# Optimization experiments

Hardware: AMD Instinct MI355X
Metric: run time of the kernel (lower is better)

The kernel has to match this reference:

```python
import jax, jax.numpy as jnp
import numpy as np

D_MODEL = 512
WINDOW_SIZE = 257


def setup_inputs() -> dict:
    key = jax.random.key(0)
    ks = jax.random.split(key, 7)
    B, S, D = 4, 4096, D_MODEL
    scale = 1.0 / np.sqrt(D)
    return {
        "x": jax.random.normal(ks[0], (B, S, D), dtype=jnp.float32),
        "Wq": jax.random.normal(ks[1], (D, D), dtype=jnp.float32) * scale,
        "bq": jnp.zeros((D,), dtype=jnp.float32),
        "Wk": jax.random.normal(ks[2], (D, D), dtype=jnp.float32) * scale,
        "bk": jnp.zeros((D,), dtype=jnp.float32),
        "Wv": jax.random.normal(ks[3], (D, D), dtype=jnp.float32) * scale,
        "bv": jnp.zeros((D,), dtype=jnp.float32),
    }


def reference(x, Wq, bq, Wk, bk, Wv, bv):
    B, S, D = x.shape
    half_window = (WINDOW_SIZE - 1) // 2
    Q = x @ Wq + bq
    K = x @ Wk + bk
    V = x @ Wv + bv
    # full [B,S,S] scores, then band mask |i-j| <= half_window (matches original)
    scores = jnp.einsum("bsd,btd->bst", Q, K) / jnp.sqrt(jnp.asarray(D, x.dtype))
    idx = jnp.arange(S)
    local_mask = jnp.abs(idx[:, None] - idx[None, :]) <= half_window  # [S,S]
    scores = jnp.where(local_mask[None], scores, -jnp.inf)
    attn = jax.nn.softmax(scores, axis=-1)
    return jnp.einsum("bst,btd->bsd", attn, V)
```

## Files before the change

### kernel.cpp

```cpp
#include <hip/hip_runtime.h>
#include <hip/hip_bf16.h>

#define S_LEN   4096
#define D_MOD   512
#define BATCH   4
#define HALF_W  128
#define M_TOT   (BATCH * S_LEN)

typedef __attribute__((ext_vector_type(8))) short bf16x8;
typedef __attribute__((ext_vector_type(4))) float f32x4;

__device__ __forceinline__ unsigned short f2bf(float f) {
    unsigned int u = __float_as_uint(f);
    unsigned int r = (u + 0x7fffu + ((u >> 16) & 1u)) >> 16;
    return (unsigned short)r;
}

__device__ __forceinline__ void async_copy16(const void* g, void* l) {
    __builtin_amdgcn_global_load_lds(
        (const __attribute__((address_space(1))) void*)g,
        (__attribute__((address_space(3))) void*)l, 16, 0, 0);
}

__global__ __launch_bounds__(256) void convert_xw(const float* __restrict__ x,
                                                  const float* __restrict__ Wq,
                                                  const float* __restrict__ Wk,
                                                  const float* __restrict__ Wv,
                                                  unsigned short* __restrict__ xb,
                                                  unsigned short* __restrict__ Wt) {
    __shared__ float sT[64][65];
    const int t = threadIdx.x;
    const int bid = blockIdx.x;
    if (bid < 8192) {
        int i = (bid * 256 + t) * 4;
        float4 v = *(const float4*)(x + i);
        ushort4 o;
        o.x = f2bf(v.x); o.y = f2bf(v.y); o.z = f2bf(v.z); o.w = f2bf(v.w);
        *(ushort4*)(xb + i) = o;
        return;
    }
    const int j = bid - 8192;
    const int w = j >> 6;
    const int rj = j & 63;
    const float* W = (w == 0) ? Wq : ((w == 1) ? Wk : Wv);
    const int n0 = (rj & 7) * 64, k0 = (rj >> 3) * 64;
    const int r = t >> 4, c4 = (t & 15) * 4;
    #pragma unroll
    for (int i = 0; i < 4; ++i) {
        float4 v = *(const float4*)(W + (size_t)(k0 + r + i * 16) * 512 + n0 + c4);
        sT[c4 + 0][r + i * 16] = v.x;
        sT[c4 + 1][r + i * 16] = v.y;
        sT[c4 + 2][r + i * 16] = v.z;
        sT[c4 + 3][r + i * 16] = v.w;
    }
    __syncthreads();
    #pragma unroll
    for (int i = 0; i < 4; ++i) {
        int rr = (t >> 4) + i * 16;
        ushort4 o;
        o.x = f2bf(sT[rr][c4 + 0]);
        o.y = f2bf(sT[rr][c4 + 1]);
        o.z = f2bf(sT[rr][c4 + 2]);
        o.w = f2bf(sT[rr][c4 + 3]);
        *(ushort4*)(Wt + (size_t)w * 262144 + (size_t)(n0 + rr) * 512 + k0 + c4) = o;
    }
}

__global__ __launch_bounds__(512, 1) void qkv_gemm(
    const unsigned short* __restrict__ xb, const unsigned short* __restrict__ Wt,
    const float* __restrict__ bq, const float* __restrict__ bk, const float* __restrict__ bv,
    unsigned short* __restrict__ Qo, unsigned short* __restrict__ Ko,
    unsigned short* __restrict__ Vt) {
    __shared__ __align__(16) char gsmem[98304];
    unsigned short* const sA0 = (unsigned short*)gsmem;
    unsigned short* const sA1 = (unsigned short*)(gsmem + 32768);
    unsigned short* const sB0 = (unsigned short*)(gsmem + 65536);
    unsigned short* const sB1 = (unsigned short*)(gsmem + 81920);
    unsigned short* const sT  = (unsigned short*)gsmem;

    const int t = threadIdx.x;
    const int p = blockIdx.x;
    const int l = (p & 7) * 96 + (p >> 3);
    const int mi = l / 12;
    const int rzn = l - mi * 12;
    const int wsel = rzn >> 2;
    const int ni = rzn & 3;
    const int m0 = mi * 256;
    const int n0 = ni * 128;
    const unsigned short* Wb = Wt + (size_t)wsel * 262144;

    const int w = t >> 6, lane = t & 63;
    const int wm = (w & 3) * 64, wn = (w >> 2) * 64;
    const int qd = lane >> 4, l16 = lane & 15;

    f32x4 acc[4][4] = {};

    #pragma unroll
    for (int i = 0; i < 4; ++i) {
        int c = i * 512 + t;
        int row = c >> 3, cc = c & 7;
        int g = cc ^ (row & 7);
        async_copy16(xb + (size_t)(m0 + row) * 512 + g * 8, sA0 + c * 8);
    }
    #pragma unroll
    for (int i = 0; i < 2; ++i) {
        int c = i * 512 + t;
        int row = c >> 3, cc = c & 7;
        int g = cc ^ (row & 7);
        async_copy16(Wb + (size_t)(n0 + row) * 512 + g * 8, sB0 + c * 8);
    }
    __syncthreads();

    int cur = 0;
    for (int k0 = 0; k0 < 512; k0 += 64) {
        if (k0 + 64 < 512) {
            unsigned short* dA = cur ? sA0 : sA1;
            unsigned short* dB = cur ? sB0 : sB1;
            int k0n = k0 + 64;
            #pragma unroll
            for (int i = 0; i < 4; ++i) {
                int c = i * 512 + t;
                int row = c >> 3, cc = c & 7;
                int g = cc ^ (row & 7);
                async_copy16(xb + (size_t)(m0 + row) * 512 + k0n + g * 8, dA + c * 8);
            }
            #pragma unroll
            for (int i = 0; i < 2; ++i) {
                int c = i * 512 + t;
                int row = c >> 3, cc = c & 7;
                int g = cc ^ (row & 7);
                async_copy16(Wb + (size_t)(n0 + row) * 512 + k0n + g * 8, dB + c * 8);
            }
        }

        const unsigned short* sA = cur ? sA1 : sA0;
        const unsigned short* sB = cur ? sB1 : sB0;
        #pragma unroll
        for (int ks = 0; ks < 2; ++ks) {
            bf16x8 af[4], bfr[4];
            #pragma unroll
            for (int i = 0; i < 4; ++i) {
                int row = wm + i * 16 + l16;
                int ch = (ks * 4 + qd) ^ (row & 7);
                af[i] = *(const bf16x8*)(sA + row * 64 + ch * 8);
            }
            #pragma unroll
            for (int j = 0; j < 4; ++j) {
                int row = wn + j * 16 + l16;
                int ch = (ks * 4 + qd) ^ (row & 7);
                bfr[j] = *(const bf16x8*)(sB + row * 64 + ch * 8);
            }
            #pragma unroll
            for (int i = 0; i < 4; ++i)
                #pragma unroll
                for (int j = 0; j < 4; ++j)
                    acc[i][j] = __builtin_amdgcn_mfma_f32_16x16x32_bf16(af[i], bfr[j], acc[i][j], 0, 0, 0);
        }

        __syncthreads();
        cur ^= 1;
    }

    const float* bias = (wsel == 0) ? bq : ((wsel == 1) ? bk : bv);

    if (wsel < 2) {
        #pragma unroll
        for (int j = 0; j < 4; ++j) {
            int n = wn + j * 16 + l16;
            float bj = bias[n0 + n];
            #pragma unroll
            for (int i = 0; i < 4; ++i) {
                int mb = wm + i * 16 + qd * 4;
                #pragma unroll
                for (int r = 0; r < 4; ++r)
                    sT[(mb + r) * 136 + n] = f2bf(acc[i][j][r] + bj);
            }
        }
        __syncthreads();
        unsigned short* Og = (wsel == 0) ? Qo : Ko;
        #pragma unroll
        for (int i2 = 0; i2 < 4; ++i2)
            #pragma unroll
            for (int i3 = 0; i3 < 2; ++i3) {
                int m = i2 * 64 + (t >> 3);
                int ch = (t & 7) + i3 * 8;
                bf16x8 v = *(const bf16x8*)(sT + m * 136 + ch * 8);
                *(bf16x8*)(Og + (size_t)(m0 + m) * 512 + n0 + ch * 8) = v;
            }
    } else {
        #pragma unroll
        for (int j = 0; j < 4; ++j) {
            int n = wn + j * 16 + l16;
            float bj = bias[n0 + n];
            #pragma unroll
            for (int i = 0; i < 4; ++i) {
                int mb = wm + i * 16 + qd * 4;
                #pragma unroll
                for (int r = 0; r < 4; ++r)
                    sT[n * 264 + mb + r] = f2bf(acc[i][j][r] + bj);
            }
        }
        __syncthreads();
        #pragma unroll
        for (int i2 = 0; i2 < 2; ++i2)
            #pragma unroll
            for (int i3 = 0; i3 < 4; ++i3) {
                int n = i2 * 64 + (t >> 3);
                int ch = (t & 7) + i3 * 8;
                bf16x8 v = *(const bf16x8*)(sT + n * 264 + ch * 8);
                *(bf16x8*)(Vt + (size_t)(n0 + n) * M_TOT + m0 + ch * 8) = v;
            }
    }
}

__global__ __launch_bounds__(512, 2) void attn(const unsigned short* __restrict__ Qg,
                                               const unsigned short* __restrict__ Kg,
                                               const unsigned short* __restrict__ Vt,
                                               float* __restrict__ out) {
    __shared__ __align__(16) char smem[137472];
    unsigned short* const bK0 = (unsigned short*)(smem);
    unsigned short* const bK1 = (unsigned short*)(smem + 66048);
    unsigned short* const bV0 = (unsigned short*)(smem + 33280);
    unsigned short* const bV1 = (unsigned short*)(smem + 99328);
    unsigned short* const sQ  = (unsigned short*)(smem + 66048);
    unsigned short* const sP  = (unsigned short*)(smem + 132096);
    float* const lsum = (float*)(smem + 137216);

    const int t = threadIdx.x;
    const int p = blockIdx.x;
    const int l = (p & 7) * 32 + (p >> 3);
    const int q0 = (l & 63) * 64;
    const int b = l >> 6;
    const int bS = b * S_LEN;

    const int w = t >> 6, lane = t & 63;
    const int qd = lane >> 4, l16 = lane & 15;
    const int qs = w >> 1;
    const int qh = qs * 16;
    const int kh = (w & 1) * 16;
    const int dh = (w & 1) * 256;

    if (t < 64) lsum[t] = 0.f;

    const int kt_lo = (q0 < 128) ? ((128 - q0) >> 5) : 0;
    int kt_hi = (4192 - q0) >> 5;
    if (kt_hi > 9) kt_hi = 9;

    bf16x8 qreg[16];
    f32x4 oacc[16] = {};

    {
        int key0 = q0 - HALF_W + kt_lo * 32;
        #pragma unroll
        for (int i = 0; i < 4; ++i) {
            int c = i * 512 + t;
            int row = c >> 6, cc = c & 63;
            int rowg = key0 + row;
            rowg = (rowg < 0) ? 0 : ((rowg > S_LEN - 1) ? S_LEN - 1 : rowg);
            async_copy16(Kg + (size_t)(bS + rowg) * 512 + cc * 8, bK0 + row * 520 + cc * 8);
        }
        #pragma unroll
        for (int i = 0; i < 4; ++i) {
            int c = i * 512 + t;
            int rp = c >> 3, chs = c & 7;
            int ch = chs ^ (rp & 7);
            int d = rp * 2 + (ch >> 2);
            int kc = ch & 3;
            int kk = key0 + kc * 8;
            int koff = (kk >= 0 && kk + 8 <= S_LEN) ? kk : 0;
            async_copy16(Vt + (size_t)d * M_TOT + bS + koff, bV0 + c * 8);
        }
        #pragma unroll
        for (int i = 0; i < 8; ++i) {
            int c = i * 512 + t;
            int row = c >> 6, cc = c & 63;
            int g = cc ^ (row & 7);
            async_copy16(Qg + (size_t)(bS + q0 + row) * 512 + g * 8, sQ + row * 512 + cc * 8);
        }
    }
    asm volatile("s_waitcnt vmcnt(0)" ::: "memory");
    __builtin_amdgcn_s_barrier();
    #pragma unroll
    for (int c4 = 0; c4 < 4; ++c4)
        #pragma unroll
        for (int kc = 0; kc < 4; ++kc) {
            int chl = c4 * 16 + kc * 4 + qd;
            int chp = chl ^ (l16 & 7);
            qreg[c4 * 4 + kc] = *(const bf16x8*)(sQ + (qh + l16) * 512 + chp * 8);
        }
    asm volatile("s_waitcnt lgkmcnt(0)" ::: "memory");
    __builtin_amdgcn_s_barrier();

    int cur = 0;
    for (int kt = kt_lo; kt <= kt_hi; ++kt, cur ^= 1) {
        const int key0 = q0 - HALF_W + kt * 32;

        asm volatile("s_waitcnt vmcnt(0) lgkmcnt(0)" ::: "memory");
        __builtin_amdgcn_s_barrier();

        if (kt < kt_hi) {
            int key0n = key0 + 32;
            unsigned short* dK = cur ? bK0 : bK1;
            unsigned short* dV = cur ? bV0 : bV1;
            #pragma unroll
            for (int i = 0; i < 4; ++i) {
                int c = i * 512 + t;
                int row = c >> 6, cc = c & 63;
                int rowg = key0n + row;
                rowg = (rowg < 0) ? 0 : ((rowg > S_LEN - 1) ? S_LEN - 1 : rowg);
                async_copy16(Kg + (size_t)(bS + rowg) * 512 + cc * 8, dK + row * 520 + cc * 8);
            }
            #pragma unroll
            for (int i = 0; i < 4; ++i) {
                int c = i * 512 + t;
                int rp = c >> 3, chs = c & 7;
                int ch = chs ^ (rp & 7);
                int d = rp * 2 + (ch >> 2);
                int kc = ch & 3;
                int kk = key0n + kc * 8;
                int koff = (kk >= 0 && kk + 8 <= S_LEN) ? kk : 0;
                async_copy16(Vt + (size_t)d * M_TOT + bS + koff, dV + c * 8);
            }
        }

        const unsigned short* sK = cur ? bK1 : bK0;
        const unsigned short* sV = cur ? bV1 : bV0;

        f32x4 sacc = {0.f, 0.f, 0.f, 0.f};
        #pragma unroll
        for (int c4 = 0; c4 < 4; ++c4) {
            #pragma unroll
            for (int kc = 0; kc < 4; ++kc) {
                bf16x8 bk8 = *(const bf16x8*)(sK + (kh + l16) * 520 + c4 * 128 + kc * 32 + qd * 8);
                sacc = __builtin_amdgcn_mfma_f32_16x16x32_bf16(qreg[c4 * 4 + kc], bk8, sacc, 0, 0, 0);
            }
        }
        const float scale = 0.04419417382415922f;
        #pragma unroll
        for (int r = 0; r < 4; ++r) {
            int qi = q0 + qh + qd * 4 + r;
            int kj = key0 + kh + l16;
            bool valid = (kj >= 0) && (kj < S_LEN) && (kj >= qi - HALF_W) && (kj <= qi + HALF_W);
            float p2 = valid ? __expf(sacc[r] * scale) : 0.f;
            sP[(qh + qd * 4 + r) * 40 + kh + l16] = f2bf(p2);
            float s = p2;
            s += __shfl_xor(s, 1);
            s += __shfl_xor(s, 2);
            s += __shfl_xor(s, 4);
            s += __shfl_xor(s, 8);
            if (l16 == 0) atomicAdd(&lsum[qh + qd * 4 + r], s);
        }

        asm volatile("s_waitcnt lgkmcnt(0)" ::: "memory");
        __builtin_amdgcn_s_barrier();

        bf16x8 ap = *(const bf16x8*)(sP + (qh + l16) * 40 + qd * 8);
        #pragma unroll
        for (int dt = 0; dt < 16; ++dt) {
            int dv = dh + dt * 16 + l16;
            int rp = dv >> 1;
            int chs = (((dv & 1) << 2) + qd) ^ (rp & 7);
            bf16x8 bv8 = *(const bf16x8*)(sV + rp * 64 + chs * 8);
            oacc[dt] = __builtin_amdgcn_mfma_f32_16x16x32_bf16(ap, bv8, oacc[dt], 0, 0, 0);
        }
    }

    asm volatile("s_waitcnt lgkmcnt(0)" ::: "memory");
    __builtin_amdgcn_s_barrier();

    float inv[4];
    #pragma unroll
    for (int r = 0; r < 4; ++r)
        inv[r] = 1.0f / lsum[qh + qd * 4 + r];

    #pragma unroll
    for (int dt = 0; dt < 16; ++dt) {
        int dv = dh + dt * 16 + l16;
        #pragma unroll
        for (int r = 0; r < 4; ++r) {
            int q = qh + qd * 4 + r;
            out[(size_t)(bS + q0 + q) * 512 + dv] = oacc[dt][r] * inv[r];
        }
    }
}

extern "C" void kernel_launch(void* const* d_in, const int* in_sizes, int n_in,
                              void* d_out, int out_size, void* d_ws, size_t ws_size,
                              hipStream_t stream) {
    const float* x  = (const float*)d_in[0];
    const float* Wq = (const float*)d_in[1];
    const float* bq = (const float*)d_in[2];
    const float* Wk = (const float*)d_in[3];
    const float* bk = (const float*)d_in[4];
    const float* Wv = (const float*)d_in[5];
    const float* bv = (const float*)d_in[6];
    float* out = (float*)d_out;

    char* ws = (char*)d_ws;
    unsigned short* xb = (unsigned short*)(ws);
    unsigned short* Wt = (unsigned short*)(ws + 16777216);
    unsigned short* Qb = (unsigned short*)(ws + 18350080);
    unsigned short* Kb = (unsigned short*)(ws + 35127296);
    unsigned short* Vt = (unsigned short*)(ws + 51904512);

    convert_xw<<<8384, 256, 0, stream>>>(x, Wq, Wk, Wv, xb, Wt);
    qkv_gemm<<<768, 512, 0, stream>>>(xb, Wt, bq, bk, bv, Qb, Kb, Vt);
    attn<<<256, 512, 0, stream>>>(Qb, Kb, Vt, out);
}
```

Before: 157.3 us.

## Stage K/V tiles through registers with two-ahead prefetch instead of async LDS loads

Replaces the direct global-to-LDS async copies of K and V tiles with ordinary global loads into registers, which are then written to the alternate LDS buffer after each tile's compute. The prefetch now runs two tiles ahead, and the barrier moves to the end of the loop iteration. The aim is to hide global load latency behind the QK and PV MFMA work. In exchange it adds register pressure (8 extra bf16x8 vectors alongside 16 accumulators and 16 Q registers), explicit LDS store instructions, and reliance on compiler-inserted vmcnt waits.

```diff
diff --git a/kernel.cpp b/kernel.cpp
--- a/kernel.cpp
+++ b/kernel.cpp
@@ -246,8 +246,9 @@
     int kt_hi = (4192 - q0) >> 5;
     if (kt_hi > 9) kt_hi = 9;
 
-    bf16x8 qreg[16];
+    bf16x8 qreg[16], kreg[4], vreg[4];
     f32x4 oacc[16] = {};
+
 
     {
         int key0 = q0 - HALF_W + kt_lo * 32;
@@ -257,7 +258,7 @@
             int row = c >> 6, cc = c & 63;
             int rowg = key0 + row;
             rowg = (rowg < 0) ? 0 : ((rowg > S_LEN - 1) ? S_LEN - 1 : rowg);
-            async_copy16(Kg + (size_t)(bS + rowg) * 512 + cc * 8, bK0 + row * 520 + cc * 8);
+            kreg[i] = *(const bf16x8*)(Kg + (size_t)(bS + rowg) * 512 + cc * 8);
         }
         #pragma unroll
         for (int i = 0; i < 4; ++i) {
@@ -268,7 +269,7 @@
             int kc = ch & 3;
             int kk = key0 + kc * 8;
             int koff = (kk >= 0 && kk + 8 <= S_LEN) ? kk : 0;
-            async_copy16(Vt + (size_t)d * M_TOT + bS + koff, bV0 + c * 8);
+            vreg[i] = *(const bf16x8*)(Vt + (size_t)d * M_TOT + bS + koff);
         }
         #pragma unroll
         for (int i = 0; i < 8; ++i) {
@@ -291,38 +292,45 @@
     asm volatile("s_waitcnt lgkmcnt(0)" ::: "memory");
     __builtin_amdgcn_s_barrier();
 
+    #pragma unroll
+    for (int i = 0; i < 4; ++i) {
+        int c = i * 512 + t;
+        int row = c >> 6, cc = c & 63;
+        *(bf16x8*)(bK0 + row * 520 + cc * 8) = kreg[i];
+    }
+    #pragma unroll
+    for (int i = 0; i < 4; ++i) {
+        int c = i * 512 + t;
+        *(bf16x8*)(bV0 + c * 8) = vreg[i];
+    }
+    {
+        int key0n = q0 - HALF_W + (kt_lo + 1) * 32;
+        #pragma unroll
+        for (int i = 0; i < 4; ++i) {
+            int c = i * 512 + t;
+            int row = c >> 6, cc = c & 63;
+            int rowg = key0n + row;
+            rowg = (rowg < 0) ? 0 : ((rowg > S_LEN - 1) ? S_LEN - 1 : rowg);
+            kreg[i] = *(const bf16x8*)(Kg + (size_t)(bS + rowg) * 512 + cc * 8);
+        }
+        #pragma unroll
+        for (int i = 0; i < 4; ++i) {
+            int c = i * 512 + t;
+            int rp = c >> 3, chs = c & 7;
+            int ch = chs ^ (rp & 7);
+            int d = rp * 2 + (ch >> 2);
+            int kc = ch & 3;
+            int kk = key0n + kc * 8;
+            int koff = (kk >= 0 && kk + 8 <= S_LEN) ? kk : 0;
+            vreg[i] = *(const bf16x8*)(Vt + (size_t)d * M_TOT + bS + koff);
+        }
+    }
+    asm volatile("s_waitcnt lgkmcnt(0)" ::: "memory");
+    __builtin_amdgcn_s_barrier();
+
     int cur = 0;
     for (int kt = kt_lo; kt <= kt_hi; ++kt, cur ^= 1) {
         const int key0 = q0 - HALF_W + kt * 32;
-
-        asm volatile("s_waitcnt vmcnt(0) lgkmcnt(0)" ::: "memory");
-        __builtin_amdgcn_s_barrier();
-
-        if (kt < kt_hi) {
-            int key0n = key0 + 32;
-            unsigned short* dK = cur ? bK0 : bK1;
-            unsigned short* dV = cur ? bV0 : bV1;
-            #pragma unroll
-            for (int i = 0; i < 4; ++i) {
-                int c = i * 512 + t;
-                int row = c >> 6, cc = c & 63;
-                int rowg = key0n + row;
-                rowg = (rowg < 0) ? 0 : ((rowg > S_LEN - 1) ? S_LEN - 1 : rowg);
-                async_copy16(Kg + (size_t)(bS + rowg) * 512 + cc * 8, dK + row * 520 + cc * 8);
-            }
-            #pragma unroll
-            for (int i = 0; i < 4; ++i) {
-                int c = i * 512 + t;
-                int rp = c >> 3, chs = c & 7;
-                int ch = chs ^ (rp & 7);
-                int d = rp * 2 + (ch >> 2);
-                int kc = ch & 3;
-                int kk = key0n + kc * 8;
-                int koff = (kk >= 0 && kk + 8 <= S_LEN) ? kk : 0;
-                async_copy16(Vt + (size_t)d * M_TOT + bS + koff, dV + c * 8);
-            }
-        }
-
         const unsigned short* sK = cur ? bK1 : bK0;
         const unsigned short* sV = cur ? bV1 : bV0;
 
@@ -363,10 +371,49 @@
             bf16x8 bv8 = *(const bf16x8*)(sV + rp * 64 + chs * 8);
             oacc[dt] = __builtin_amdgcn_mfma_f32_16x16x32_bf16(ap, bv8, oacc[dt], 0, 0, 0);
         }
-    }
-
-    asm volatile("s_waitcnt lgkmcnt(0)" ::: "memory");
-    __builtin_amdgcn_s_barrier();
+
+        if (kt < kt_hi) {
+            unsigned short* dK = cur ? bK0 : bK1;
+            unsigned short* dV = cur ? bV0 : bV1;
+            asm volatile("s_waitcnt vmcnt(0)" ::: "memory");
+            #pragma unroll
+            for (int i = 0; i < 4; ++i) {
+                int c = i * 512 + t;
+                int row = c >> 6, cc = c & 63;
+                *(bf16x8*)(dK + row * 520 + cc * 8) = kreg[i];
+            }
+            #pragma unroll
+            for (int i = 0; i < 4; ++i) {
+                int c = i * 512 + t;
+                *(bf16x8*)(dV + c * 8) = vreg[i];
+            }
+            if (kt + 2 <= kt_hi) {
+                int key0n = key0 + 64;
+                #pragma unroll
+                for (int i = 0; i < 4; ++i) {
+                    int c = i * 512 + t;
+                    int row = c >> 6, cc = c & 63;
+                    int rowg = key0n + row;
+                    rowg = (rowg < 0) ? 0 : ((rowg > S_LEN - 1) ? S_LEN - 1 : rowg);
+                    kreg[i] = *(const bf16x8*)(Kg + (size_t)(bS + rowg) * 512 + cc * 8);
+                }
+                #pragma unroll
+                for (int i = 0; i < 4; ++i) {
+                    int c = i * 512 + t;
+                    int rp = c >> 3, chs = c & 7;
+                    int ch = chs ^ (rp & 7);
+                    int d = rp * 2 + (ch >> 2);
+                    int kc = ch & 3;
+                    int kk = key0n + kc * 8;
+                    int koff = (kk >= 0 && kk + 8 <= S_LEN) ? kk : 0;
+                    vreg[i] = *(const bf16x8*)(Vt + (size_t)d * M_TOT + bS + koff);
+                }
+            }
+        }
+
+        asm volatile("s_waitcnt lgkmcnt(0)" ::: "memory");
+        __builtin_amdgcn_s_barrier();
+    }
 
     float inv[4];
     #pragma unroll
```

Measured after the change: 162.1 us. 1.03x slower.

## Software-pipeline attention loop: overlap QK^T of tile i with PV of tile i-1

Applied to the files above, without the earlier changes.

Restructures the key-tile loop into a skewed pipeline. Each iteration computes scores and probabilities for tile i while doing the P·V product for tile i-1, using double-buffered P tiles. K is prefetched one tile ahead and V is loaded one iteration before it is consumed. This drops one barrier per iteration and lets the score MFMAs/exp interleave with the PV MFMAs, at the cost of slightly more LDS (second P buffer) and an extra loop iteration.

```diff
diff --git a/kernel.cpp b/kernel.cpp
--- a/kernel.cpp
+++ b/kernel.cpp
@@ -217,14 +217,15 @@
                                                const unsigned short* __restrict__ Kg,
                                                const unsigned short* __restrict__ Vt,
                                                float* __restrict__ out) {
-    __shared__ __align__(16) char smem[137472];
-    unsigned short* const bK0 = (unsigned short*)(smem);
-    unsigned short* const bK1 = (unsigned short*)(smem + 66048);
-    unsigned short* const bV0 = (unsigned short*)(smem + 33280);
-    unsigned short* const bV1 = (unsigned short*)(smem + 99328);
-    unsigned short* const sQ  = (unsigned short*)(smem + 66048);
-    unsigned short* const sP  = (unsigned short*)(smem + 132096);
-    float* const lsum = (float*)(smem + 137216);
+    __shared__ __align__(16) char smem[142592];
+    unsigned short* const K0 = (unsigned short*)(smem);
+    unsigned short* const K1 = (unsigned short*)(smem + 33280);
+    unsigned short* const V0 = (unsigned short*)(smem + 66560);
+    unsigned short* const V1 = (unsigned short*)(smem + 99328);
+    unsigned short* const sQ = (unsigned short*)(smem + 66560);
+    unsigned short* const P0 = (unsigned short*)(smem + 132096);
+    unsigned short* const P1 = (unsigned short*)(smem + 137216);
+    float* const lsum = (float*)(smem + 142336);
 
     const int t = threadIdx.x;
     const int p = blockIdx.x;
@@ -235,8 +236,7 @@
 
     const int w = t >> 6, lane = t & 63;
     const int qd = lane >> 4, l16 = lane & 15;
-    const int qs = w >> 1;
-    const int qh = qs * 16;
+    const int qh = (w >> 1) * 16;
     const int kh = (w & 1) * 16;
     const int dh = (w & 1) * 256;
 
@@ -249,16 +249,17 @@
     bf16x8 qreg[16];
     f32x4 oacc[16] = {};
 
-    {
-        int key0 = q0 - HALF_W + kt_lo * 32;
+    auto stageK = [&](int key0, unsigned short* dst) {
         #pragma unroll
         for (int i = 0; i < 4; ++i) {
             int c = i * 512 + t;
             int row = c >> 6, cc = c & 63;
             int rowg = key0 + row;
             rowg = (rowg < 0) ? 0 : ((rowg > S_LEN - 1) ? S_LEN - 1 : rowg);
-            async_copy16(Kg + (size_t)(bS + rowg) * 512 + cc * 8, bK0 + row * 520 + cc * 8);
-        }
+            async_copy16(Kg + (size_t)(bS + rowg) * 512 + cc * 8, dst + row * 520 + cc * 8);
+        }
+    };
+    auto stageV = [&](int key0, unsigned short* dst) {
         #pragma unroll
         for (int i = 0; i < 4; ++i) {
             int c = i * 512 + t;
@@ -268,15 +269,17 @@
             int kc = ch & 3;
             int kk = key0 + kc * 8;
             int koff = (kk >= 0 && kk + 8 <= S_LEN) ? kk : 0;
-            async_copy16(Vt + (size_t)d * M_TOT + bS + koff, bV0 + c * 8);
-        }
-        #pragma unroll
-        for (int i = 0; i < 8; ++i) {
-            int c = i * 512 + t;
-            int row = c >> 6, cc = c & 63;
-            int g = cc ^ (row & 7);
-            async_copy16(Qg + (size_t)(bS + q0 + row) * 512 + g * 8, sQ + row * 512 + cc * 8);
-        }
+            async_copy16(Vt + (size_t)d * M_TOT + bS + koff, dst + c * 8);
+        }
+    };
+
+    stageK(q0 - HALF_W + kt_lo * 32, (kt_lo & 1) ? K1 : K0);
+    #pragma unroll
+    for (int i = 0; i < 8; ++i) {
+        int c = i * 512 + t;
+        int row = c >> 6, cc = c & 63;
+        int g = cc ^ (row & 7);
+        async_copy16(Qg + (size_t)(bS + q0 + row) * 512 + g * 8, sQ + row * 512 + cc * 8);
     }
     asm volatile("s_waitcnt vmcnt(0)" ::: "memory");
     __builtin_amdgcn_s_barrier();
@@ -291,81 +294,62 @@
     asm volatile("s_waitcnt lgkmcnt(0)" ::: "memory");
     __builtin_amdgcn_s_barrier();
 
-    int cur = 0;
-    for (int kt = kt_lo; kt <= kt_hi; ++kt, cur ^= 1) {
-        const int key0 = q0 - HALF_W + kt * 32;
-
-        asm volatile("s_waitcnt vmcnt(0) lgkmcnt(0)" ::: "memory");
+    const float scale = 0.04419417382415922f;
+
+    for (int i = kt_lo; i <= kt_hi + 1; ++i) {
+        const int key0 = q0 - HALF_W + i * 32;
+
+        asm volatile("s_waitcnt vmcnt(0)" ::: "memory");
         __builtin_amdgcn_s_barrier();
-
-        if (kt < kt_hi) {
-            int key0n = key0 + 32;
-            unsigned short* dK = cur ? bK0 : bK1;
-            unsigned short* dV = cur ? bV0 : bV1;
-            #pragma unroll
-            for (int i = 0; i < 4; ++i) {
-                int c = i * 512 + t;
-                int row = c >> 6, cc = c & 63;
-                int rowg = key0n + row;
-                rowg = (rowg < 0) ? 0 : ((rowg > S_LEN - 1) ? S_LEN - 1 : rowg);
-                async_copy16(Kg + (size_t)(bS + rowg) * 512 + cc * 8, dK + row * 520 + cc * 8);
-            }
-            #pragma unroll
-            for (int i = 0; i < 4; ++i) {
-                int c = i * 512 + t;
-                int rp = c >> 3, chs = c & 7;
-                int ch = chs ^ (rp & 7);
-                int d = rp * 2 + (ch >> 2);
-                int kc = ch & 3;
-                int kk = key0n + kc * 8;
-                int koff = (kk >= 0 && kk + 8 <= S_LEN) ? kk : 0;
-                async_copy16(Vt + (size_t)d * M_TOT + bS + koff, dV + c * 8);
-            }
-        }
-
-        const unsigned short* sK = cur ? bK1 : bK0;
-        const unsigned short* sV = cur ? bV1 : bV0;
-
-        f32x4 sacc = {0.f, 0.f, 0.f, 0.f};
-        #pragma unroll
-        for (int c4 = 0; c4 < 4; ++c4) {
-            #pragma unroll
-            for (int kc = 0; kc < 4; ++kc) {
-                bf16x8 bk8 = *(const bf16x8*)(sK + (kh + l16) * 520 + c4 * 128 + kc * 32 + qd * 8);
-                sacc = __builtin_amdgcn_mfma_f32_16x16x32_bf16(qreg[c4 * 4 + kc], bk8, sacc, 0, 0, 0);
-            }
-        }
-        const float scale = 0.04419417382415922f;
-        #pragma unroll
-        for (int r = 0; r < 4; ++r) {
-            int qi = q0 + qh + qd * 4 + r;
-            int kj = key0 + kh + l16;
-            bool valid = (kj >= 0) && (kj < S_LEN) && (kj >= qi - HALF_W) && (kj <= qi + HALF_W);
-            float p2 = valid ? __expf(sacc[r] * scale) : 0.f;
-            sP[(qh + qd * 4 + r) * 40 + kh + l16] = f2bf(p2);
-            float s = p2;
-            s += __shfl_xor(s, 1);
-            s += __shfl_xor(s, 2);
-            s += __shfl_xor(s, 4);
-            s += __shfl_xor(s, 8);
-            if (l16 == 0) atomicAdd(&lsum[qh + qd * 4 + r], s);
+        __builtin_amdgcn_sched_barrier(0);
+
+        if (i + 1 <= kt_hi) stageK(key0 + 32, ((i + 1) & 1) ? K1 : K0);
+        if (i <= kt_hi)     stageV(key0,      (i & 1) ? V1 : V0);
+
+        if (i <= kt_hi) {
+            const unsigned short* sK = (i & 1) ? K1 : K0;
+            f32x4 sacc = {0.f, 0.f, 0.f, 0.f};
+            #pragma unroll
+            for (int c4 = 0; c4 < 4; ++c4) {
+                #pragma unroll
+                for (int kc = 0; kc < 4; ++kc) {
+                    bf16x8 bk8 = *(const bf16x8*)(sK + (kh + l16) * 520 + c4 * 128 + kc * 32 + qd * 8);
+                    sacc = __builtin_amdgcn_mfma_f32_16x16x32_bf16(qreg[c4 * 4 + kc], bk8, sacc, 0, 0, 0);
+                }
+            }
+            unsigned short* sPc = (i & 1) ? P1 : P0;
+            #pragma unroll
+            for (int r = 0; r < 4; ++r) {
+                int qi = q0 + qh + qd * 4 + r;
+                int kj = key0 + kh + l16;
+                bool valid = (kj >= 0) && (kj < S_LEN) && (kj >= qi - HALF_W) && (kj <= qi + HALF_W);
+                float p2 = valid ? __expf(sacc[r] * scale) : 0.f;
+                sPc[(qh + qd * 4 + r) * 40 + kh + l16] = f2bf(p2);
+                float s = p2;
+                s += __shfl_xor(s, 1);
+                s += __shfl_xor(s, 2);
+                s += __shfl_xor(s, 4);
+                s += __shfl_xor(s, 8);
+                if (l16 == 0) atomicAdd(&lsum[qh + qd * 4 + r], s);
+            }
+        }
+
+        if (i > kt_lo) {
+            const unsigned short* sV  = ((i - 1) & 1) ? V1 : V0;
+            const unsigned short* sPp = ((i - 1) & 1) ? P1 : P0;
+            bf16x8 ap = *(const bf16x8*)(sPp + (qh + l16) * 40 + qd * 8);
+            #pragma unroll
+            for (int dt = 0; dt < 16; ++dt) {
+                int dv = dh + dt * 16 + l16;
+                int rp = dv >> 1;
+                int chs = (((dv & 1) << 2) + qd) ^ (rp & 7);
+                bf16x8 bv8 = *(const bf16x8*)(sV + rp * 64 + chs * 8);
+                oacc[dt] = __builtin_amdgcn_mfma_f32_16x16x32_bf16(ap, bv8, oacc[dt], 0, 0, 0);
+            }
         }
 
         asm volatile("s_waitcnt lgkmcnt(0)" ::: "memory");
-        __builtin_amdgcn_s_barrier();
-
-        bf16x8 ap = *(const bf16x8*)(sP + (qh + l16) * 40 + qd * 8);
-        #pragma unroll
-        for (int dt = 0; dt < 16; ++dt) {
-            int dv = dh + dt * 16 + l16;
-            int rp = dv >> 1;
-            int chs = (((dv & 1) << 2) + qd) ^ (rp & 7);
-            bf16x8 bv8 = *(const bf16x8*)(sV + rp * 64 + chs * 8);
-            oacc[dt] = __builtin_amdgcn_mfma_f32_16x16x32_bf16(ap, bv8, oacc[dt], 0, 0, 0);
-        }
-    }
-
-    asm volatile("s_waitcnt lgkmcnt(0)" ::: "memory");
+    }
     __builtin_amdgcn_s_barrier();
 
     float inv[4];
```

After: 157.1 us. Within noise of the previous version (-0.1%).
